# Performance work log

Hardware: AMD Instinct MI355X
Metric: run time of the kernel (lower is better)

## Reference

```python
import jax, jax.numpy as jnp
import numpy as np

B, T, E, H = 4, 2048, 1024, 16
HS = E // H  # head_size = 64
FFN_HID = 100  # hard-coded in FeedForward
EPS = 1e-5


def layernorm(x, g, b):
    mu = jnp.mean(x, axis=-1, keepdims=True)
    var = jnp.mean(jnp.square(x - mu), axis=-1, keepdims=True)
    return (x - mu) * jax.lax.rsqrt(var + EPS) * g + b


def setup_inputs() -> dict:
    key = jax.random.key(0)
    ks = jax.random.split(key, 10)
    s = E ** -0.5
    return {
        "x": jax.random.normal(ks[0], (B, T, E), jnp.float32),
        "wq": jax.random.normal(ks[1], (E, E), jnp.float32) * s,
        "wk": jax.random.normal(ks[2], (E, E), jnp.float32) * s,
        "wv": jax.random.normal(ks[3], (E, E), jnp.float32) * s,
        "w_proj": jax.random.normal(ks[4], (E, E), jnp.float32) * s,
        "b_proj": jnp.zeros((E,), jnp.float32),
        "w1": jax.random.normal(ks[5], (E, FFN_HID), jnp.float32) * s,
        "b1": jnp.zeros((FFN_HID,), jnp.float32),
        "w2": jax.random.normal(ks[6], (FFN_HID, E), jnp.float32) * (FFN_HID ** -0.5),
        "b2": jnp.zeros((E,), jnp.float32),
        "ln1_g": jnp.ones((E,), jnp.float32),
        "ln1_b": jnp.zeros((E,), jnp.float32),
        "ln2_g": jnp.ones((E,), jnp.float32),
        "ln2_b": jnp.zeros((E,), jnp.float32),
    }


def reference(x, wq, wk, wv, w_proj, b_proj, w1, b1, w2, b2, ln1_g, ln1_b, ln2_g, ln2_b):
    # --- self-attention with pre-LN residual ---
    h = layernorm(x, ln1_g, ln1_b)  # [B,T,E]
    def split_heads(y):  # [B,T,E] -> [B,H,T,HS]
        return y.reshape(B, T, H, HS).transpose(0, 2, 1, 3)
    q = split_heads(h @ wq)
    k = split_heads(h @ wk)
    v = split_heads(h @ wv)
    # NOTE: original scales by C**-0.5 with C = n_embd (not head_size)
    wei = jnp.einsum("bhtd,bhsd->bhts", q, k) * (E ** -0.5)  # [B,H,T,T]
    causal = jnp.tril(jnp.ones((T, T), bool))
    wei = jnp.where(causal, wei, -jnp.inf)
    wei = jax.nn.softmax(wei, axis=-1)
    att = jnp.einsum("bhts,bhsd->bhtd", wei, v)  # [B,H,T,HS]
    att = att.transpose(0, 2, 1, 3).reshape(B, T, E)  # concat heads
    x = x + att @ w_proj + b_proj
    # --- feedforward with pre-LN residual ---
    h2 = layernorm(x, ln2_g, ln2_b)
    ff = jax.nn.relu(h2 @ w1 + b1) @ w2 + b2
    return x + ff
```

## Files before the change

kernel.cpp:

```cpp
#include <hip/hip_runtime.h>

typedef unsigned short u16;
typedef unsigned int u32;
typedef __bf16 bf16x8 __attribute__((ext_vector_type(8)));
typedef float f32x4 __attribute__((ext_vector_type(4)));

#define BDIM 4
#define TDIM 2048
#define EDIM 1024
#define HDIM 16
#define HS 64
#define MROWS (BDIM * TDIM)
#define FFNP 128

__device__ __forceinline__ u16 f2bf(float f) {
    __bf16 h = (__bf16)f;
    return __builtin_bit_cast(u16, h);
}

__device__ __forceinline__ void glds16(const void* g, void* l) {
    __builtin_amdgcn_global_load_lds(
        (__attribute__((address_space(1))) const void*)g,
        (__attribute__((address_space(3))) void*)l, 16, 0, 0);
}

__global__ __launch_bounds__(256) void transpose4(
    const float* __restrict__ s0, const float* __restrict__ s1,
    const float* __restrict__ s2, const float* __restrict__ s3,
    u16* __restrict__ d0, u16* __restrict__ d1,
    u16* __restrict__ d2, u16* __restrict__ d3)
{
    __shared__ u16 sm[64][72];
    const float* src; u16* dst;
    switch (blockIdx.z) {
        case 0: src = s0; dst = d0; break;
        case 1: src = s1; dst = d1; break;
        case 2: src = s2; dst = d2; break;
        default: src = s3; dst = d3; break;
    }
    int k0 = blockIdx.x * 64, n0 = blockIdx.y * 64;
    int tid = threadIdx.x;
#pragma unroll
    for (int i = 0; i < 16; i++) {
        int idx = i * 256 + tid;
        int kl = idx >> 6, nl = idx & 63;
        sm[kl][nl] = f2bf(src[(size_t)(k0 + kl) * EDIM + n0 + nl]);
    }
    __syncthreads();
#pragma unroll
    for (int i = 0; i < 16; i++) {
        int idx = i * 256 + tid;
        int nl = idx >> 6, kl = idx & 63;
        dst[(size_t)(n0 + nl) * EDIM + k0 + kl] = sm[kl][nl];
    }
}

__global__ __launch_bounds__(256) void transpose_pad(
    const float* __restrict__ src, u16* __restrict__ dst,
    int K, int N, int Kpad, int Npad)
{
    __shared__ u16 sm[64][72];
    int k0 = blockIdx.x * 64, n0 = blockIdx.y * 64;
    int tid = threadIdx.x;
#pragma unroll
    for (int i = 0; i < 16; i++) {
        int idx = i * 256 + tid;
        int kl = idx >> 6, nl = idx & 63;
        int k = k0 + kl, n = n0 + nl;
        float v = (k < K && n < N) ? src[(size_t)k * N + n] : 0.f;
        sm[kl][nl] = f2bf(v);
    }
    __syncthreads();
#pragma unroll
    for (int i = 0; i < 16; i++) {
        int idx = i * 256 + tid;
        int nl = idx >> 6, kl = idx & 63;
        int n = n0 + nl, k = k0 + kl;
        if (n < Npad && k < Kpad) dst[(size_t)n * Kpad + k] = sm[kl][nl];
    }
}

__global__ __launch_bounds__(256) void ln_rows(
    const float* __restrict__ X, const float* __restrict__ G,
    const float* __restrict__ Bv, u16* __restrict__ H)
{
    int w = threadIdx.x >> 6, l = threadIdx.x & 63;
    int row = blockIdx.x * 4 + w;
    const float* xr = X + (size_t)row * EDIM;
    float4 v[4];
    float s = 0.f, s2 = 0.f;
#pragma unroll
    for (int i = 0; i < 4; i++) {
        v[i] = *(const float4*)&xr[l * 4 + i * 256];
        s += v[i].x + v[i].y + v[i].z + v[i].w;
        s2 += v[i].x * v[i].x + v[i].y * v[i].y + v[i].z * v[i].z + v[i].w * v[i].w;
    }
#pragma unroll
    for (int off = 1; off < 64; off <<= 1) {
        s += __shfl_xor(s, off, 64);
        s2 += __shfl_xor(s2, off, 64);
    }
    float mean = s * (1.f / EDIM);
    float var = s2 * (1.f / EDIM) - mean * mean;
    float rstd = rsqrtf(var + 1e-5f);
#pragma unroll
    for (int i = 0; i < 4; i++) {
        int c = l * 4 + i * 256;
        float4 gg = *(const float4*)&G[c];
        float4 bb = *(const float4*)&Bv[c];
        u16 o0 = f2bf((v[i].x - mean) * rstd * gg.x + bb.x);
        u16 o1 = f2bf((v[i].y - mean) * rstd * gg.y + bb.y);
        u16 o2 = f2bf((v[i].z - mean) * rstd * gg.z + bb.z);
        u16 o3 = f2bf((v[i].w - mean) * rstd * gg.w + bb.w);
        uint2 pk;
        pk.x = (u32)o0 | ((u32)o1 << 16);
        pk.y = (u32)o2 | ((u32)o3 << 16);
        *(uint2*)&H[(size_t)row * EDIM + c] = pk;
    }
}

#define LDA4(d, mfb)                                                          \
    _Pragma("unroll") for (int mi = 0; mi < 4; mi++)                          \
    _Pragma("unroll") for (int ks = 0; ks < 2; ks++)                          \
        a[mi][ks] = *(const bf16x8*)&L[d][0][wm][((mfb + mi) * 16 + lr) * 64  \
                        + (((lg + 4 * ks) ^ (lr & 7)) << 3)];
#define LDB2(d, nfb)                                                          \
    _Pragma("unroll") for (int ni = 0; ni < 2; ni++)                          \
    _Pragma("unroll") for (int ks = 0; ks < 2; ks++)                          \
        b[ni][ks] = *(const bf16x8*)&L[d][1][wh][((wn & 1) * 64               \
                        + (nfb + ni) * 16 + lr) * 64                          \
                        + (((lg + 4 * ks) ^ (lr & 7)) << 3)];
#define MFMAQ(mfb, nfb)                                                       \
    _Pragma("unroll") for (int mi = 0; mi < 4; mi++)                          \
    _Pragma("unroll") for (int ni = 0; ni < 2; ni++)                          \
    _Pragma("unroll") for (int ks = 0; ks < 2; ks++)                          \
        acc[mfb + mi][nfb + ni] = __builtin_amdgcn_mfma_f32_16x16x32_bf16(    \
            a[mi][ks], b[ni][ks], acc[mfb + mi][nfb + ni], 0, 0, 0);
#define PH_SYNC1()                                                            \
    __builtin_amdgcn_s_barrier();                                             \
    asm volatile("s_waitcnt lgkmcnt(0)" ::: "memory");                        \
    __builtin_amdgcn_sched_barrier(0);                                        \
    __builtin_amdgcn_s_setprio(1);
#define PH_SYNC2()                                                            \
    __builtin_amdgcn_s_setprio(0);                                            \
    __builtin_amdgcn_s_barrier();
#define PH_SYNC2V(cond)                                                       \
    __builtin_amdgcn_s_setprio(0);                                            \
    if (cond) { asm volatile("s_waitcnt vmcnt(2)" ::: "memory"); }            \
    else      { asm volatile("s_waitcnt vmcnt(0)" ::: "memory"); }            \
    __builtin_amdgcn_s_barrier();

template <int MODE>
__global__ __launch_bounds__(512, 2) void gemm256(
    const u16* __restrict__ A, const u16* __restrict__ Bt,
    u16* __restrict__ Cb, float* __restrict__ Cf,
    const float* __restrict__ resid, const float* __restrict__ bias,
    int M, int N, int K, int lda, int ldb, int mb)
{
    __shared__ u16 L[2][2][2][128 * 64];
    const u16 *pA, *pB;
    int LA, LB, NN, bx, by;
    bool vmode = false;
    if constexpr (MODE == 5) {
        int id = blockIdx.x;
        if (id < 256) {
            int sw = (id & 7) * 32 + (id >> 3);
            bx = sw % 32; by = sw / 32;
            pA = A; pB = Bt; LA = 1024; LB = 1024; NN = 2048;
        } else {
            id -= 256;
            int sw = (id & 7) * 16 + (id >> 3);
            bx = sw % 4; by = sw / 4;
            pA = Bt + (size_t)2048 * 1024;
            pB = A;
            LA = 1024; LB = 1024; NN = 8192;
            vmode = true;
        }
    } else {
        int nwg = gridDim.x, id = blockIdx.x;
        int sw = (id & 7) * (nwg >> 3) + (id >> 3);
        bx = sw % mb; by = sw / mb;
        pA = A; pB = Bt; LA = lda; LB = ldb; NN = N;
    }
    const int m0 = bx * 256, n0 = by * 256;

    const int tid = threadIdx.x;
    const int w = tid >> 6, l = tid & 63;
    const int wm = w >> 2, wn = w & 3, wh = wn >> 1;
    const int lg = l >> 4, lr = l & 15;

    const int srow = w * 16 + (l >> 3);
    const int sch8 = ((l & 7) ^ (l >> 3)) * 8;

    auto stA = [&](int d, int h, int t) {
        const u16* src = pA + (size_t)(m0 + h * 128 + srow) * LA + t * 64 + sch8;
        u16* dst = &L[d][0][h][w * 1024];
        glds16(src, dst);
        glds16(src + (size_t)8 * LA, dst + 512);
    };
    auto stB = [&](int d, int h, int t) {
        const u16* src = pB + (size_t)(n0 + h * 128 + srow) * LB + t * 64 + sch8;
        u16* dst = &L[d][1][h][w * 1024];
        glds16(src, dst);
        glds16(src + (size_t)8 * LB, dst + 512);
    };

    f32x4 acc[8][4];
#pragma unroll
    for (int i = 0; i < 8; i++)
#pragma unroll
        for (int j = 0; j < 4; j++) acc[i][j] = f32x4{0.f, 0.f, 0.f, 0.f};
    bf16x8 a[4][2], b[2][2];

    const int NI = K >> 7;

    stA(0, 0, 0); stA(0, 1, 0); stB(0, 0, 0); stB(0, 1, 0);
    stB(1, 0, 1);
    asm volatile("s_waitcnt vmcnt(2)" ::: "memory");
    __builtin_amdgcn_s_barrier();

#pragma unroll 1
    for (int j = 0; j < NI; j++) {
        const int t = 2 * j;
        const bool more = (j + 1 < NI);
        LDA4(0, 0); LDB2(0, 0);
        stA(1, 0, t + 1);
        PH_SYNC1(); MFMAQ(0, 0); PH_SYNC2();
        LDA4(0, 4);
        stA(1, 1, t + 1);
        PH_SYNC1(); MFMAQ(4, 0); PH_SYNC2();
        LDB2(0, 2);
        stB(1, 1, t + 1);
        PH_SYNC1(); MFMAQ(4, 2); PH_SYNC2();
        LDA4(0, 0);
        if (more) stB(0, 1, t + 2);
        PH_SYNC1(); MFMAQ(0, 2); PH_SYNC2V(more);
        LDA4(1, 0); LDB2(1, 0);
        if (more) stA(0, 0, t + 2);
        PH_SYNC1(); MFMAQ(0, 0); PH_SYNC2();
        LDA4(1, 4);
        if (more) stA(0, 1, t + 2);
        PH_SYNC1(); MFMAQ(4, 0); PH_SYNC2();
        LDB2(1, 2);
        if (more) stB(0, 0, t + 2);
        PH_SYNC1(); MFMAQ(4, 2); PH_SYNC2();
        LDA4(1, 0);
        if (more) stB(1, 0, t + 3);
        PH_SYNC1(); MFMAQ(0, 2); PH_SYNC2V(more);
    }

#pragma unroll
    for (int mf = 0; mf < 8; mf++) {
#pragma unroll
        for (int nf = 0; nf < 4; nf++) {
#pragma unroll
            for (int e = 0; e < 4; e++) {
                int row = m0 + wm * 128 + mf * 16 + lg * 4 + e;
                int col = n0 + wn * 64 + nf * 16 + lr;
                float v = acc[mf][nf][e];
                if constexpr (MODE == 5) {
                    if (!vmode) {
                        Cb[(size_t)row * 2048 + col] = f2bf(v);
                    } else {
                        u16* vtp = (u16*)Cf;
                        int bq = col >> 11, tt = col & 2047;
                        vtp[((size_t)bq * 1024 + row) * 2048 + tt] = f2bf(v);
                    }
                } else {
                    size_t idx = (size_t)row * NN + col;
                    Cf[idx] = resid[idx] + v + bias[col];
                }
            }
        }
    }
}

template <int MODE>
__global__ __launch_bounds__(256, 2) void gemm_bt(
    const u16* __restrict__ A, const u16* __restrict__ Bt,
    u16* __restrict__ Cb, float* __restrict__ Cf,
    const float* __restrict__ resid, const float* __restrict__ bias,
    int M, int N, int K, int lda, int ldb, int mb)
{
    __shared__ u16 As[2][128 * 32];
    __shared__ u16 Bs[2][128 * 32];
    int bx, by;
    if constexpr (MODE == 4) {
        bx = blockIdx.x; by = blockIdx.y;
        int kz = blockIdx.z;
        A += kz * 256;
        Bt += kz * 256;
        Cf += (size_t)kz * M * N;
    } else {
        int nwg = gridDim.x, id = blockIdx.x;
        int sw = (id & 7) * (nwg >> 3) + (id >> 3);
        bx = sw % mb; by = sw / mb;
    }
    const int tid = threadIdx.x;
    const int w = tid >> 6, l = tid & 63;
    const int wr = w >> 1, wc = w & 1;
    const int lg = l >> 4, lr = l & 15;
    const int m0 = bx * 128, n0 = by * 128;

    f32x4 zero = {0.f, 0.f, 0.f, 0.f};
    f32x4 acc[4][4];
#pragma unroll
    for (int i = 0; i < 4; i++)
#pragma unroll
        for (int j = 0; j < 4; j++) acc[i][j] = zero;

    const u16* Ag = A + (size_t)(m0 + w * 16 + (l >> 2)) * lda + (l & 3) * 8;
    const u16* Bg = Bt + (size_t)(n0 + w * 16 + (l >> 2)) * ldb + (l & 3) * 8;

    auto stage = [&](int b, int k0) {
        glds16(Ag + k0, &As[b][w * 512]);
        glds16(Ag + k0 + (size_t)64 * lda, &As[b][w * 512 + 2048]);
        glds16(Bg + k0, &Bs[b][w * 512]);
        glds16(Bg + k0 + (size_t)64 * ldb, &Bs[b][w * 512 + 2048]);
    };
    auto compute = [&](int b) {
        bf16x8 af[4], bfr[4];
#pragma unroll
        for (int t = 0; t < 4; t++)
            af[t] = *(const bf16x8*)&As[b][(wr * 64 + t * 16 + lr) * 32 + lg * 8];
#pragma unroll
        for (int t = 0; t < 4; t++)
            bfr[t] = *(const bf16x8*)&Bs[b][(wc * 64 + t * 16 + lr) * 32 + lg * 8];
#pragma unroll
        for (int i = 0; i < 4; i++)
#pragma unroll
            for (int j = 0; j < 4; j++)
                acc[i][j] = __builtin_amdgcn_mfma_f32_16x16x32_bf16(
                    af[i], bfr[j], acc[i][j], 0, 0, 0);
    };

    stage(0, 0);
    __syncthreads();
    int cur = 0;
    for (int k0 = 32; k0 < K; k0 += 32) {
        stage(cur ^ 1, k0);
        compute(cur);
        __syncthreads();
        cur ^= 1;
    }
    compute(cur);

#pragma unroll
    for (int i = 0; i < 4; i++) {
#pragma unroll
        for (int j = 0; j < 4; j++) {
#pragma unroll
            for (int e = 0; e < 4; e++) {
                int row = m0 + wr * 64 + i * 16 + lg * 4 + e;
                int col = n0 + wc * 64 + j * 16 + lr;
                float v = acc[i][j][e];
                size_t idx = (size_t)row * N + col;
                if constexpr (MODE == 3) {
                    Cf[idx] = resid[idx] + v + bias[col];
                } else {
                    Cf[idx] = v;
                }
            }
        }
    }
}

__global__ __launch_bounds__(256) void relu_reduce4(
    const float* __restrict__ fp, const float* __restrict__ b1,
    u16* __restrict__ tb)
{
    const size_t CH = (size_t)MROWS * FFNP;
    size_t base = ((size_t)blockIdx.x * 256 + threadIdx.x) * 4;
    float4 s0 = *(const float4*)&fp[base];
    float4 s1 = *(const float4*)&fp[base + CH];
    float4 s2 = *(const float4*)&fp[base + 2 * CH];
    float4 s3 = *(const float4*)&fp[base + 3 * CH];
    int col = (int)(base & (FFNP - 1));
    float sv[4] = {s0.x + s1.x + s2.x + s3.x, s0.y + s1.y + s2.y + s3.y,
                   s0.z + s1.z + s2.z + s3.z, s0.w + s1.w + s2.w + s3.w};
    u16 o[4];
#pragma unroll
    for (int j = 0; j < 4; j++) {
        int c = col + j;
        float b = (c < 100) ? b1[c] : 0.f;
        o[j] = f2bf(fmaxf(sv[j] + b, 0.f));
    }
    uint2 pk;
    pk.x = (u32)o[0] | ((u32)o[1] << 16);
    pk.y = (u32)o[2] | ((u32)o[3] << 16);
    *(uint2*)&tb[base] = pk;
}

__global__ __launch_bounds__(256, 4) void attn_fwd(
    const u16* __restrict__ qk, const u16* __restrict__ Vt,
    u16* __restrict__ Og)
{
    int xcd = blockIdx.x & 7;
    int j = blockIdx.x >> 3;
    int bh = xcd * 8 + (j & 7);
    int qp = j >> 3;
    int bb = bh >> 4, hh = bh & 15;

    int tid = threadIdx.x;
    int w = tid >> 6, l = tid & 63;
    int lg = l >> 4, lr = l & 15;

    const u16* Qb = qk + ((size_t)bb * TDIM) * 2048 + hh * HS;
    const u16* Kb = Qb + 1024;
    const u16* Vb = Vt + (size_t)bh * HS * TDIM;

    __shared__ u16 Ks[2][64 * 64];
    __shared__ u16 Vs[2][64 * 64];
    __shared__ u16 Ps[4][16 * 64];

    int srow = w * 16 + (l >> 3);
    int schunk = (l & 7) ^ ((l >> 3) & 7);
    u16* Pw = Ps[w];
    int sbase = (l & 48) + lg * 4;

    const float QSCL = 0.045084227f;

#pragma unroll 1
    for (int qi = 0; qi < 2; qi++) {
        int qb = (qi == 0 ? qp : 31 - qp) * 64;
        int q_abs = qb + w * 16 + lr;
        int wlo = qb + w * 16;
        int nt = qb / 64 + 1;

        bf16x8 qf[2];
        qf[0] = *(const bf16x8*)&Qb[(size_t)q_abs * 2048 + lg * 8];
        qf[1] = *(const bf16x8*)&Qb[(size_t)q_abs * 2048 + 32 + lg * 8];
#pragma unroll
        for (int i = 0; i < 8; i++) {
            qf[0][i] = (__bf16)((float)qf[0][i] * QSCL);
            qf[1][i] = (__bf16)((float)qf[1][i] * QSCL);
        }

        f32x4 zero = {0.f, 0.f, 0.f, 0.f};
        f32x4 oacc[4];
#pragma unroll
        for (int dt = 0; dt < 4; dt++) oacc[dt] = zero;
        float lpart = 0.f;

        auto stage = [&](int b, int kv0) {
            glds16(Kb + (size_t)(kv0 + srow) * 2048 + schunk * 8, &Ks[b][w * 1024]);
            glds16(Kb + (size_t)(kv0 + srow + 8) * 2048 + schunk * 8,
                   &Ks[b][w * 1024 + 512]);
            glds16(Vb + (size_t)srow * TDIM + kv0 + schunk * 8, &Vs[b][w * 1024]);
            glds16(Vb + (size_t)(srow + 8) * TDIM + kv0 + schunk * 8,
                   &Vs[b][w * 1024 + 512]);
        };

        stage(0, 0);
        __syncthreads();
        int cur = 0;
#pragma unroll 1
        for (int t = 0; t < nt; t++) {
            int kv0 = t * 64;
            if (t + 1 < nt) stage(cur ^ 1, kv0 + 64);
            const u16* Kc = Ks[cur];
            const u16* Vc = Vs[cur];
            f32x4 sc[4];
#pragma unroll
            for (int ct = 0; ct < 4; ct++) sc[ct] = zero;
            __builtin_amdgcn_s_setprio(1);
#pragma unroll
            for (int ct = 0; ct < 4; ct++) {
#pragma unroll
                for (int dc = 0; dc < 2; dc++) {
                    bf16x8 kf = *(const bf16x8*)&Kc[(ct * 16 + lr) * 64 +
                                                    (((lg + 4 * dc) ^ (lr & 7)) << 3)];
                    sc[ct] = __builtin_amdgcn_mfma_f32_16x16x32_bf16(
                        kf, qf[dc], sc[ct], 0, 0, 0);
                }
            }
            __builtin_amdgcn_s_setprio(0);
            bf16x8 vfr[2][4];
#pragma unroll
            for (int m = 0; m < 2; m++)
#pragma unroll
                for (int dt = 0; dt < 4; dt++)
                    vfr[m][dt] = *(const bf16x8*)&Vc[(dt * 16 + lr) * 64 +
                                                     (((lg + 4 * m) ^ (lr & 7)) << 3)];
            float p[16];
            if (kv0 + 63 > wlo) {
#pragma unroll
                for (int ct = 0; ct < 4; ct++) {
#pragma unroll
                    for (int e = 0; e < 4; e++) {
                        float v = sc[ct][e];
                        if (kv0 + ct * 16 + lg * 4 + e > q_abs) v = -1e30f;
                        p[ct * 4 + e] = v;
                    }
                }
            } else {
#pragma unroll
                for (int ct = 0; ct < 4; ct++) {
#pragma unroll
                    for (int e = 0; e < 4; e++) p[ct * 4 + e] = sc[ct][e];
                }
            }
            float psum = 0.f;
#pragma unroll
            for (int i = 0; i < 16; i++) {
                p[i] = __builtin_amdgcn_exp2f(p[i]);
                psum += p[i];
            }
            lpart += psum;
#pragma unroll
            for (int ct = 0; ct < 4; ct++) {
#pragma unroll
                for (int i = 0; i < 2; i++) {
                    u32 word = (u32)f2bf(p[ct * 4 + 2 * i]) |
                               ((u32)f2bf(p[ct * 4 + 2 * i + 1]) << 16);
                    int kvb = ct * 16 + lg * 4 + 2 * i;
                    int idx = lr * 64 + ((((kvb >> 3) ^ (lr & 7)) << 3) | (kvb & 7));
                    *(u32*)&Pw[idx] = word;
                }
            }
            asm volatile("s_waitcnt lgkmcnt(0)" ::: "memory");
            __builtin_amdgcn_sched_barrier(0);
            __builtin_amdgcn_s_setprio(1);
#pragma unroll
            for (int m = 0; m < 2; m++) {
                bf16x8 pa = *(const bf16x8*)&Pw[lr * 64 + (((lg + 4 * m) ^ (lr & 7)) << 3)];
#pragma unroll
                for (int dt = 0; dt < 4; dt++) {
                    oacc[dt] = __builtin_amdgcn_mfma_f32_16x16x32_bf16(
                        pa, vfr[m][dt], oacc[dt], 0, 0, 0);
                }
            }
            __builtin_amdgcn_s_setprio(0);
            __syncthreads();
            cur ^= 1;
        }
        float lsum = lpart;
        lsum += __shfl_xor(lsum, 16, 64);
        lsum += __shfl_xor(lsum, 32, 64);
        float lT[4];
#pragma unroll
        for (int e = 0; e < 4; e++) lT[e] = __shfl(lsum, sbase + e, 64);
#pragma unroll
        for (int dt = 0; dt < 4; dt++) {
#pragma unroll
            for (int e = 0; e < 4; e++) {
                int row = qb + w * 16 + lg * 4 + e;
                Og[((size_t)bb * TDIM + row) * EDIM + hh * HS + dt * 16 + lr] =
                    f2bf(oacc[dt][e] / lT[e]);
            }
        }
    }
}

extern "C" void kernel_launch(void* const* d_in, const int* in_sizes, int n_in,
                              void* d_out, int out_size, void* d_ws, size_t ws_size,
                              hipStream_t stream)
{
    const float* x     = (const float*)d_in[0];
    const float* wq    = (const float*)d_in[1];
    const float* wk    = (const float*)d_in[2];
    const float* wv    = (const float*)d_in[3];
    const float* wproj = (const float*)d_in[4];
    const float* bproj = (const float*)d_in[5];
    const float* w1    = (const float*)d_in[6];
    const float* b1    = (const float*)d_in[7];
    const float* w2    = (const float*)d_in[8];
    const float* b2    = (const float*)d_in[9];
    const float* ln1g  = (const float*)d_in[10];
    const float* ln1b  = (const float*)d_in[11];
    const float* ln2g  = (const float*)d_in[12];
    const float* ln2b  = (const float*)d_in[13];
    float* out = (float*)d_out;

    char* ws = (char*)d_ws;
    size_t off = 0;
    auto alloc = [&](size_t bytes) -> void* {
        void* p = (void*)(ws + off);
        off += (bytes + 255) & ~(size_t)255;
        return p;
    };
    u16* hbuf = (u16*)alloc((size_t)MROWS * EDIM * 2);
    u16* qk   = (u16*)alloc((size_t)MROWS * 2048 * 2);
    u16* attb = (u16*)alloc((size_t)MROWS * EDIM * 2);
    u16* vt   = (u16*)alloc((size_t)MROWS * EDIM * 2);
    u16* wqkvt = (u16*)alloc((size_t)3072 * EDIM * 2);
    u16* wpt  = (u16*)alloc((size_t)EDIM * EDIM * 2);
    u16* w1t  = (u16*)alloc((size_t)FFNP * EDIM * 2);
    u16* w2t  = (u16*)alloc((size_t)EDIM * FFNP * 2);
    float* fp = (float*)qk;
    u16* tb   = vt;

    transpose4<<<dim3(16, 16, 4), 256, 0, stream>>>(
        wq, wk, wv, wproj,
        wqkvt, wqkvt + (size_t)EDIM * EDIM, wqkvt + (size_t)2 * EDIM * EDIM, wpt);
    transpose_pad<<<dim3(16, 2), 256, 0, stream>>>(w1, w1t, EDIM, 100, EDIM, FFNP);
    transpose_pad<<<dim3(2, 16), 256, 0, stream>>>(w2, w2t, 100, EDIM, FFNP, EDIM);

    ln_rows<<<MROWS / 4, 256, 0, stream>>>(x, ln1g, ln1b, hbuf);
    gemm256<5><<<dim3(384), 512, 0, stream>>>(hbuf, wqkvt, qk, (float*)vt,
                                              nullptr, nullptr,
                                              MROWS, 2048, EDIM, EDIM, EDIM, 32);
    attn_fwd<<<dim3(1024), 256, 0, stream>>>(qk, vt, attb);
    gemm256<1><<<dim3(128), 512, 0, stream>>>(attb, wpt, nullptr, out, x, bproj,
                                              MROWS, EDIM, EDIM, EDIM, EDIM, 32);
    ln_rows<<<MROWS / 4, 256, 0, stream>>>(out, ln2g, ln2b, hbuf);
    gemm_bt<4><<<dim3(64, 1, 4), 256, 0, stream>>>(hbuf, w1t, nullptr, fp, nullptr,
                                                   nullptr, MROWS, FFNP, 256, EDIM, EDIM, 64);
    relu_reduce4<<<dim3(MROWS * FFNP / 1024), 256, 0, stream>>>(fp, b1, tb);
    gemm_bt<3><<<dim3(512), 256, 0, stream>>>(tb, w2t, nullptr, out, out, b2,
                                              MROWS, EDIM, FFNP, FFNP, FFNP, 64);
}
```

Before: 236.5 us.

## Merge weight transposes, move proj GEMM to gemm_bt, deepen attention KV prefetch

Three weight-transpose launches become one kernel, with out-of-range blocks returning early. The output projection moves from the 256x256-tile gemm256 (128 workgroups) to gemm_bt with 512 workgroups, aiming at better CU occupancy. The QKV GEMM is specialized with constant strides. In attention, K/V staging now prefetches two tiles ahead, synchronized with vmcnt waits and raw barriers instead of __syncthreads, to overlap loads with compute; this relies on correct wait counts.

```diff
diff --git a/kernel.cpp b/kernel.cpp
--- a/kernel.cpp
+++ b/kernel.cpp
@@ -24,43 +24,26 @@
         (__attribute__((address_space(3))) void*)l, 16, 0, 0);
 }
 
-__global__ __launch_bounds__(256) void transpose4(
-    const float* __restrict__ s0, const float* __restrict__ s1,
-    const float* __restrict__ s2, const float* __restrict__ s3,
-    u16* __restrict__ d0, u16* __restrict__ d1,
-    u16* __restrict__ d2, u16* __restrict__ d3)
+__global__ __launch_bounds__(256) void transpose_all(
+    const float* __restrict__ wq, const float* __restrict__ wk,
+    const float* __restrict__ wv, const float* __restrict__ wproj,
+    const float* __restrict__ w1, const float* __restrict__ w2,
+    u16* __restrict__ wqkvt, u16* __restrict__ wpt,
+    u16* __restrict__ w1t, u16* __restrict__ w2t)
 {
     __shared__ u16 sm[64][72];
     const float* src; u16* dst;
+    int K, N, Kpad, Npad;
     switch (blockIdx.z) {
-        case 0: src = s0; dst = d0; break;
-        case 1: src = s1; dst = d1; break;
-        case 2: src = s2; dst = d2; break;
-        default: src = s3; dst = d3; break;
+        case 0: src = wq;    dst = wqkvt;                 K = N = Kpad = Npad = 1024; break;
+        case 1: src = wk;    dst = wqkvt + 1024 * 1024;   K = N = Kpad = Npad = 1024; break;
+        case 2: src = wv;    dst = wqkvt + 2 * 1024 * 1024; K = N = Kpad = Npad = 1024; break;
+        case 3: src = wproj; dst = wpt;                   K = N = Kpad = Npad = 1024; break;
+        case 4: src = w1;    dst = w1t; K = 1024; N = 100; Kpad = 1024; Npad = 128; break;
+        default: src = w2;   dst = w2t; K = 100; N = 1024; Kpad = 128; Npad = 1024; break;
     }
     int k0 = blockIdx.x * 64, n0 = blockIdx.y * 64;
-    int tid = threadIdx.x;
-#pragma unroll
-    for (int i = 0; i < 16; i++) {
-        int idx = i * 256 + tid;
-        int kl = idx >> 6, nl = idx & 63;
-        sm[kl][nl] = f2bf(src[(size_t)(k0 + kl) * EDIM + n0 + nl]);
-    }
-    __syncthreads();
-#pragma unroll
-    for (int i = 0; i < 16; i++) {
-        int idx = i * 256 + tid;
-        int nl = idx >> 6, kl = idx & 63;
-        dst[(size_t)(n0 + nl) * EDIM + k0 + kl] = sm[kl][nl];
-    }
-}
-
-__global__ __launch_bounds__(256) void transpose_pad(
-    const float* __restrict__ src, u16* __restrict__ dst,
-    int K, int N, int Kpad, int Npad)
-{
-    __shared__ u16 sm[64][72];
-    int k0 = blockIdx.x * 64, n0 = blockIdx.y * 64;
+    if (k0 >= Kpad || n0 >= Npad) return;
     int tid = threadIdx.x;
 #pragma unroll
     for (int i = 0; i < 16; i++) {
@@ -150,37 +133,28 @@
     else      { asm volatile("s_waitcnt vmcnt(0)" ::: "memory"); }            \
     __builtin_amdgcn_s_barrier();
 
-template <int MODE>
-__global__ __launch_bounds__(512, 2) void gemm256(
+__global__ __launch_bounds__(512, 2) void gemm256_qkv(
     const u16* __restrict__ A, const u16* __restrict__ Bt,
-    u16* __restrict__ Cb, float* __restrict__ Cf,
-    const float* __restrict__ resid, const float* __restrict__ bias,
-    int M, int N, int K, int lda, int ldb, int mb)
+    u16* __restrict__ Cb, u16* __restrict__ vtp)
 {
     __shared__ u16 L[2][2][2][128 * 64];
     const u16 *pA, *pB;
-    int LA, LB, NN, bx, by;
+    int bx, by;
     bool vmode = false;
-    if constexpr (MODE == 5) {
+    {
         int id = blockIdx.x;
         if (id < 256) {
             int sw = (id & 7) * 32 + (id >> 3);
             bx = sw % 32; by = sw / 32;
-            pA = A; pB = Bt; LA = 1024; LB = 1024; NN = 2048;
+            pA = A; pB = Bt;
         } else {
             id -= 256;
             int sw = (id & 7) * 16 + (id >> 3);
             bx = sw % 4; by = sw / 4;
             pA = Bt + (size_t)2048 * 1024;
             pB = A;
-            LA = 1024; LB = 1024; NN = 8192;
             vmode = true;
         }
-    } else {
-        int nwg = gridDim.x, id = blockIdx.x;
-        int sw = (id & 7) * (nwg >> 3) + (id >> 3);
-        bx = sw % mb; by = sw / mb;
-        pA = A; pB = Bt; LA = lda; LB = ldb; NN = N;
     }
     const int m0 = bx * 256, n0 = by * 256;
 
@@ -193,16 +167,16 @@
     const int sch8 = ((l & 7) ^ (l >> 3)) * 8;
 
     auto stA = [&](int d, int h, int t) {
-        const u16* src = pA + (size_t)(m0 + h * 128 + srow) * LA + t * 64 + sch8;
+        const u16* src = pA + (size_t)(m0 + h * 128 + srow) * 1024 + t * 64 + sch8;
         u16* dst = &L[d][0][h][w * 1024];
         glds16(src, dst);
-        glds16(src + (size_t)8 * LA, dst + 512);
+        glds16(src + (size_t)8 * 1024, dst + 512);
     };
     auto stB = [&](int d, int h, int t) {
-        const u16* src = pB + (size_t)(n0 + h * 128 + srow) * LB + t * 64 + sch8;
+        const u16* src = pB + (size_t)(n0 + h * 128 + srow) * 1024 + t * 64 + sch8;
         u16* dst = &L[d][1][h][w * 1024];
         glds16(src, dst);
-        glds16(src + (size_t)8 * LB, dst + 512);
+        glds16(src + (size_t)8 * 1024, dst + 512);
     };
 
     f32x4 acc[8][4];
@@ -212,7 +186,7 @@
         for (int j = 0; j < 4; j++) acc[i][j] = f32x4{0.f, 0.f, 0.f, 0.f};
     bf16x8 a[4][2], b[2][2];
 
-    const int NI = K >> 7;
+    const int NI = 1024 >> 7;
 
     stA(0, 0, 0); stA(0, 1, 0); stB(0, 0, 0); stB(0, 1, 0);
     stB(1, 0, 1);
@@ -258,17 +232,11 @@
                 int row = m0 + wm * 128 + mf * 16 + lg * 4 + e;
                 int col = n0 + wn * 64 + nf * 16 + lr;
                 float v = acc[mf][nf][e];
-                if constexpr (MODE == 5) {
-                    if (!vmode) {
-                        Cb[(size_t)row * 2048 + col] = f2bf(v);
-                    } else {
-                        u16* vtp = (u16*)Cf;
-                        int bq = col >> 11, tt = col & 2047;
-                        vtp[((size_t)bq * 1024 + row) * 2048 + tt] = f2bf(v);
-                    }
+                if (!vmode) {
+                    Cb[(size_t)row * 2048 + col] = f2bf(v);
                 } else {
-                    size_t idx = (size_t)row * NN + col;
-                    Cf[idx] = resid[idx] + v + bias[col];
+                    int bq = col >> 11, tt = col & 2047;
+                    vtp[((size_t)bq * 1024 + row) * 2048 + tt] = f2bf(v);
                 }
             }
         }
@@ -278,7 +246,7 @@
 template <int MODE>
 __global__ __launch_bounds__(256, 2) void gemm_bt(
     const u16* __restrict__ A, const u16* __restrict__ Bt,
-    u16* __restrict__ Cb, float* __restrict__ Cf,
+    float* __restrict__ Cf,
     const float* __restrict__ resid, const float* __restrict__ bias,
     int M, int N, int K, int lda, int ldb, int mb)
 {
@@ -355,7 +323,7 @@
                 int col = n0 + wc * 64 + j * 16 + lr;
                 float v = acc[i][j][e];
                 size_t idx = (size_t)row * N + col;
-                if constexpr (MODE == 3) {
+                if constexpr (MODE == 1 || MODE == 3) {
                     Cf[idx] = resid[idx] + v + bias[col];
                 } else {
                     Cf[idx] = v;
@@ -452,14 +420,17 @@
         };
 
         stage(0, 0);
-        __syncthreads();
-        int cur = 0;
+        if (nt > 1) stage(1, 64);
 #pragma unroll 1
         for (int t = 0; t < nt; t++) {
             int kv0 = t * 64;
-            if (t + 1 < nt) stage(cur ^ 1, kv0 + 64);
-            const u16* Kc = Ks[cur];
-            const u16* Vc = Vs[cur];
+            int buf = t & 1;
+            if (t + 1 < nt) { asm volatile("s_waitcnt vmcnt(4)" ::: "memory"); }
+            else            { asm volatile("s_waitcnt vmcnt(0)" ::: "memory"); }
+            __builtin_amdgcn_sched_barrier(0);
+            __builtin_amdgcn_s_barrier();
+            const u16* Kc = Ks[buf];
+            const u16* Vc = Vs[buf];
             f32x4 sc[4];
 #pragma unroll
             for (int ct = 0; ct < 4; ct++) sc[ct] = zero;
@@ -531,8 +502,8 @@
                 }
             }
             __builtin_amdgcn_s_setprio(0);
-            __syncthreads();
-            cur ^= 1;
+            __builtin_amdgcn_s_barrier();
+            if (t + 2 < nt) stage(buf, kv0 + 128);
         }
         float lsum = lpart;
         lsum += __shfl_xor(lsum, 16, 64);
@@ -590,23 +561,18 @@
     float* fp = (float*)qk;
     u16* tb   = vt;
 
-    transpose4<<<dim3(16, 16, 4), 256, 0, stream>>>(
-        wq, wk, wv, wproj,
-        wqkvt, wqkvt + (size_t)EDIM * EDIM, wqkvt + (size_t)2 * EDIM * EDIM, wpt);
-    transpose_pad<<<dim3(16, 2), 256, 0, stream>>>(w1, w1t, EDIM, 100, EDIM, FFNP);
-    transpose_pad<<<dim3(2, 16), 256, 0, stream>>>(w2, w2t, 100, EDIM, FFNP, EDIM);
+    transpose_all<<<dim3(16, 16, 6), 256, 0, stream>>>(
+        wq, wk, wv, wproj, w1, w2, wqkvt, wpt, w1t, w2t);
 
     ln_rows<<<MROWS / 4, 256, 0, stream>>>(x, ln1g, ln1b, hbuf);
-    gemm256<5><<<dim3(384), 512, 0, stream>>>(hbuf, wqkvt, qk, (float*)vt,
-                                              nullptr, nullptr,
-                                              MROWS, 2048, EDIM, EDIM, EDIM, 32);
+    gemm256_qkv<<<dim3(384), 512, 0, stream>>>(hbuf, wqkvt, qk, vt);
     attn_fwd<<<dim3(1024), 256, 0, stream>>>(qk, vt, attb);
-    gemm256<1><<<dim3(128), 512, 0, stream>>>(attb, wpt, nullptr, out, x, bproj,
-                                              MROWS, EDIM, EDIM, EDIM, EDIM, 32);
+    gemm_bt<1><<<dim3(512), 256, 0, stream>>>(attb, wpt, out, x, bproj,
+                                              MROWS, EDIM, EDIM, EDIM, EDIM, 64);
     ln_rows<<<MROWS / 4, 256, 0, stream>>>(out, ln2g, ln2b, hbuf);
-    gemm_bt<4><<<dim3(64, 1, 4), 256, 0, stream>>>(hbuf, w1t, nullptr, fp, nullptr,
-                                                   nullptr, MROWS, FFNP, 256, EDIM, EDIM, 64);
+    gemm_bt<4><<<dim3(64, 1, 4), 256, 0, stream>>>(hbuf, w1t, fp, nullptr, nullptr,
+                                                   MROWS, FFNP, 256, EDIM, EDIM, 64);
     relu_reduce4<<<dim3(MROWS * FFNP / 1024), 256, 0, stream>>>(fp, b1, tb);
-    gemm_bt<3><<<dim3(512), 256, 0, stream>>>(tb, w2t, nullptr, out, out, b2,
+    gemm_bt<3><<<dim3(512), 256, 0, stream>>>(tb, w2t, out, out, b2,
                                               MROWS, EDIM, FFNP, FFNP, FFNP, 64);
 }
```

Measured after the change: 216.7 us. 1.09x faster.
